# Kernel optimization log

Measured on AMD Instinct MI355X. Metric: run time of the kernel, lower is better.

Reference implementation:

```python
import jax, jax.numpy as jnp
import numpy as np

N = 1048576   # total points
C = 64        # in_planes
B = 16        # number of batch segments
EPS = 1e-5    # BatchNorm eps


def setup_inputs() -> dict:
    key = jax.random.key(0)
    ks = jax.random.split(key, 10)
    x = jax.random.normal(ks[0], (N, C), dtype=jnp.float32)
    # cumulative offsets: equal-size segments, o[-1] == N
    o = (jnp.arange(1, B + 1, dtype=jnp.int32) * (N // B))
    # linear2: Linear(C, C) + ReLU
    W2 = jax.random.normal(ks[1], (C, C), dtype=jnp.float32) / np.sqrt(C)
    b2 = jax.random.normal(ks[2], (C,), dtype=jnp.float32) * 0.01
    # linear1: Linear(2C, C) + BatchNorm1d(C) + ReLU (BN in eval mode)
    W1 = jax.random.normal(ks[3], (2 * C, C), dtype=jnp.float32) / np.sqrt(2 * C)
    b1 = jax.random.normal(ks[4], (C,), dtype=jnp.float32) * 0.01
    gamma = jnp.ones((C,), dtype=jnp.float32)
    beta = jnp.zeros((C,), dtype=jnp.float32)
    run_mean = jax.random.normal(ks[5], (C,), dtype=jnp.float32) * 0.1
    run_var = jax.random.uniform(ks[6], (C,), dtype=jnp.float32, minval=0.5, maxval=1.5)
    return {"x": x, "o": o, "W2": W2, "b2": b2, "W1": W1, "b1": b1,
            "gamma": gamma, "beta": beta, "run_mean": run_mean, "run_var": run_var}


def reference(x, o, W2, b2, W1, b1, gamma, beta, run_mean, run_var):
    n = x.shape[0]
    # segment id of each point from cumulative offsets
    seg = jnp.searchsorted(o, jnp.arange(n, dtype=o.dtype), side="right")  # [N]
    counts = jnp.diff(o, prepend=jnp.zeros((1,), dtype=o.dtype))           # [B]
    # per-segment sum-pool -> mean
    sums = jax.ops.segment_sum(x, seg, num_segments=B)                     # [B, C]
    mean = sums / counts[:, None].astype(x.dtype)                          # [B, C]
    # linear2 + ReLU on the tiny [B, C] pooled features
    h = jax.nn.relu(mean @ W2 + b2)                                        # [B, C]
    # broadcast back to points and concat -> [N, 2C]
    cat = jnp.concatenate([x, h[seg]], axis=1)
    # linear1 + BatchNorm1d (eval mode) + ReLU
    z = cat @ W1 + b1                                                      # [N, C]
    z = (z - run_mean) * jax.lax.rsqrt(run_var + EPS) * gamma + beta
    return jax.nn.relu(z)
```

## Files before the change

kernel.cpp:

```cpp
#include <hip/hip_runtime.h>


#define MAXB 16

typedef _Float16 half8 __attribute__((ext_vector_type(8)));
typedef float float4v __attribute__((ext_vector_type(4)));

__global__ __launch_bounds__(256) void pool_kernel(
    const float* __restrict__ x, const int* __restrict__ o,
    float* __restrict__ gsums, int nB, int ptsPerBlock) {
  __shared__ int so_s[MAXB];
  __shared__ float red[16 * 64];
  __shared__ float ssum2[MAXB * 64];
  const int tid = threadIdx.x;
  if (tid < nB) so_s[tid] = o[tid];
  __syncthreads();

  const int c4 = (tid & 15) * 4;
  const int r  = tid >> 4;
  const int p0 = blockIdx.x * ptsPerBlock;
  const int iters = ptsPerBlock >> 4;

  int sFirst = 0;
  while (p0 >= so_s[sFirst]) sFirst++;
  int sLast = sFirst;
  while (p0 + ptsPerBlock - 1 >= so_s[sLast]) sLast++;

  if (sFirst == sLast) {
    float a0 = 0.f, a1 = 0.f, a2 = 0.f, a3 = 0.f;
    const float* xp = x + (size_t)(p0 + r) * 64 + c4;
#pragma unroll 4
    for (int i = 0; i < iters; ++i) {
      float4 v = *(const float4*)(xp + (size_t)i * 1024);
      a0 += v.x; a1 += v.y; a2 += v.z; a3 += v.w;
    }
    float4 t = {a0, a1, a2, a3};
    *(float4*)&red[r * 64 + c4] = t;
    __syncthreads();
    if (tid < 64) {
      float s = 0.f;
#pragma unroll
      for (int rr = 0; rr < 16; ++rr) s += red[rr * 64 + tid];
      atomicAdd(&gsums[sFirst * 64 + tid], s);
    }
  } else {
    for (int i = tid; i < nB * 64; i += 256) ssum2[i] = 0.f;
    __syncthreads();
    for (int i = 0; i < iters; ++i) {
      int p = p0 + i * 16 + r;
      int s = 0;
      while (p >= so_s[s]) s++;
      float4 v = *(const float4*)(x + (size_t)p * 64 + c4);
      atomicAdd(&ssum2[s * 64 + c4 + 0], v.x);
      atomicAdd(&ssum2[s * 64 + c4 + 1], v.y);
      atomicAdd(&ssum2[s * 64 + c4 + 2], v.z);
      atomicAdd(&ssum2[s * 64 + c4 + 3], v.w);
    }
    __syncthreads();
    for (int i = tid; i < nB * 64; i += 256) {
      float v = ssum2[i];
      if (v != 0.f) atomicAdd(&gsums[i], v);
    }
  }
}

__global__ __launch_bounds__(256) void mid_kernel(
    const float* __restrict__ gsums, const int* __restrict__ o,
    const float* __restrict__ W2, const float* __restrict__ b2,
    const float* __restrict__ W1, const float* __restrict__ b1,
    const float* __restrict__ gamma, const float* __restrict__ beta,
    const float* __restrict__ rmean, const float* __restrict__ rvar,
    float* __restrict__ biasp, _Float16* __restrict__ WpT, int nB) {
  __shared__ float smean[MAXB * 64];
  __shared__ float sh[MAXB * 64];
  const int tid = threadIdx.x;
  const int j = tid & 63;
  const int bq = tid >> 6;

  for (int i = tid; i < nB * 64; i += 256) {
    int b = i >> 6;
    int cnt = o[b] - (b ? o[b - 1] : 0);
    smean[i] = gsums[i] / (float)cnt;
  }
  __syncthreads();

  for (int b = bq; b < nB; b += 4) {
    float p0 = 0.f, p1 = 0.f, p2 = 0.f, p3 = 0.f;
#pragma unroll
    for (int c = 0; c < 64; c += 4) {
      p0 = fmaf(smean[b * 64 + c + 0], W2[(c + 0) * 64 + j], p0);
      p1 = fmaf(smean[b * 64 + c + 1], W2[(c + 1) * 64 + j], p1);
      p2 = fmaf(smean[b * 64 + c + 2], W2[(c + 2) * 64 + j], p2);
      p3 = fmaf(smean[b * 64 + c + 3], W2[(c + 3) * 64 + j], p3);
    }
    sh[b * 64 + j] = fmaxf(((p0 + p1) + (p2 + p3)) + b2[j], 0.f);
  }
  __syncthreads();

  const float a = gamma[j] * rsqrtf(rvar[j] + 1e-5f);
  const float d = beta[j] - rmean[j] * a;
  for (int b = bq; b < nB; b += 4) {
    float p0 = 0.f, p1 = 0.f, p2 = 0.f, p3 = 0.f;
#pragma unroll
    for (int c = 0; c < 64; c += 4) {
      p0 = fmaf(sh[b * 64 + c + 0], W1[(64 + c + 0) * 64 + j], p0);
      p1 = fmaf(sh[b * 64 + c + 1], W1[(64 + c + 1) * 64 + j], p1);
      p2 = fmaf(sh[b * 64 + c + 2], W1[(64 + c + 2) * 64 + j], p2);
      p3 = fmaf(sh[b * 64 + c + 3], W1[(64 + c + 3) * 64 + j], p3);
    }
    biasp[b * 64 + j] = (((p0 + p1) + (p2 + p3)) + b1[j]) * a + d;
  }
  for (int k = bq * 16; k < bq * 16 + 16; ++k)
    WpT[j * 64 + k] = (_Float16)(W1[k * 64 + j] * a);
}

__global__ __launch_bounds__(256) void main_kernel(
    const float* __restrict__ x, const int* __restrict__ o,
    const _Float16* __restrict__ WpT, const float* __restrict__ biasp,
    float* __restrict__ out, int nB) {
  const int lane = threadIdx.x & 63;
  const int m = lane & 15;
  const int quad = lane >> 4;
  const int rows0 = (blockIdx.x * 4 + (threadIdx.x >> 6)) * 128;

  half8 bfrag[4][2];
#pragma unroll
  for (int t = 0; t < 4; ++t)
#pragma unroll
    for (int h = 0; h < 2; ++h)
      bfrag[t][h] = *(const half8*)(WpT + (t * 16 + m) * 64 + h * 32 + quad * 8);

  const int ov = (m < nB) ? o[m] : 0x7fffffff;

  float4 f0, f1, f2, f3;
  {
    const float* p = x + (size_t)(rows0 + m) * 64 + quad * 8;
    f0 = *(const float4*)(p + 0);
    f1 = *(const float4*)(p + 4);
    f2 = *(const float4*)(p + 32);
    f3 = *(const float4*)(p + 36);
  }

  for (int i = 0; i < 8; ++i) {
    const int row0 = rows0 + i * 16;
    half8 a0, a1;
    a0[0] = (_Float16)f0.x; a0[1] = (_Float16)f0.y;
    a0[2] = (_Float16)f0.z; a0[3] = (_Float16)f0.w;
    a0[4] = (_Float16)f1.x; a0[5] = (_Float16)f1.y;
    a0[6] = (_Float16)f1.z; a0[7] = (_Float16)f1.w;
    a1[0] = (_Float16)f2.x; a1[1] = (_Float16)f2.y;
    a1[2] = (_Float16)f2.z; a1[3] = (_Float16)f2.w;
    a1[4] = (_Float16)f3.x; a1[5] = (_Float16)f3.y;
    a1[6] = (_Float16)f3.z; a1[7] = (_Float16)f3.w;

    if (i < 7) {
      const float* p = x + (size_t)(row0 + 16 + m) * 64 + quad * 8;
      f0 = *(const float4*)(p + 0);
      f1 = *(const float4*)(p + 4);
      f2 = *(const float4*)(p + 32);
      f3 = *(const float4*)(p + 36);
    }

    const int s0 = (int)__popcll(__ballot(row0 >= ov) & 0xFFFFull);
    const int s1 = (int)__popcll(__ballot(row0 + 15 >= ov) & 0xFFFFull);

    if (s0 == s1) {
      const float* bp = biasp + s0 * 64 + m;
#pragma unroll
      for (int t = 0; t < 4; ++t) {
        float4v c = {0.f, 0.f, 0.f, 0.f};
        c = __builtin_amdgcn_mfma_f32_16x16x32_f16(a0, bfrag[t][0], c, 0, 0, 0);
        c = __builtin_amdgcn_mfma_f32_16x16x32_f16(a1, bfrag[t][1], c, 0, 0, 0);
        const float bv = bp[t * 16];
        float* op = out + (size_t)(row0 + quad * 4) * 64 + t * 16 + m;
#pragma unroll
        for (int rg = 0; rg < 4; ++rg)
          op[(size_t)rg * 64] = fmaxf(c[rg] + bv, 0.f);
      }
    } else {
#pragma unroll
      for (int t = 0; t < 4; ++t) {
        float4v c = {0.f, 0.f, 0.f, 0.f};
        c = __builtin_amdgcn_mfma_f32_16x16x32_f16(a0, bfrag[t][0], c, 0, 0, 0);
        c = __builtin_amdgcn_mfma_f32_16x16x32_f16(a1, bfrag[t][1], c, 0, 0, 0);
#pragma unroll
        for (int rg = 0; rg < 4; ++rg) {
          const int row = row0 + quad * 4 + rg;
          int s = 0;
          for (int q2 = 0; q2 < nB; ++q2) s += (row >= o[q2]) ? 1 : 0;
          const float bv = biasp[s * 64 + t * 16 + m];
          out[(size_t)row * 64 + t * 16 + m] = fmaxf(c[rg] + bv, 0.f);
        }
      }
    }
  }
}

extern "C" void kernel_launch(void* const* d_in, const int* in_sizes, int n_in,
                              void* d_out, int out_size, void* d_ws, size_t ws_size,
                              hipStream_t stream) {
  const float* x     = (const float*)d_in[0];
  const int*   o     = (const int*)d_in[1];
  const float* W2    = (const float*)d_in[2];
  const float* b2    = (const float*)d_in[3];
  const float* W1    = (const float*)d_in[4];
  const float* b1    = (const float*)d_in[5];
  const float* gamma = (const float*)d_in[6];
  const float* beta  = (const float*)d_in[7];
  const float* rmean = (const float*)d_in[8];
  const float* rvar  = (const float*)d_in[9];
  float* out = (float*)d_out;

  const int npts = in_sizes[0] / 64;
  const int nB   = in_sizes[1];

  float*    gsums = (float*)d_ws;
  float*    biasp = gsums + MAXB * 64;
  _Float16* WpT   = (_Float16*)(biasp + MAXB * 64);

  hipMemsetAsync(gsums, 0, MAXB * 64 * sizeof(float), stream);

  const int blocks1 = 2048;
  pool_kernel<<<blocks1, 256, 0, stream>>>(x, o, gsums, nB, npts / blocks1);
  mid_kernel<<<1, 256, 0, stream>>>(gsums, o, W2, b2, W1, b1, gamma, beta,
                                    rmean, rvar, biasp, WpT, nB);
  main_kernel<<<npts / 512, 256, 0, stream>>>(x, o, WpT, biasp, out, nB);
}
```

Before: 524.7 us.

## Fuse pool, mid and main kernels into one persistent kernel with grid barrier

Merges the three launches into a single 512-block kernel. Each block pools its own chunk of points, then all blocks meet at a global atomic barrier. After the barrier every block redundantly computes the pooled MLP bias into shared memory, builds its own fp16 weight fragments, and then computes its rows. Because each block processes the same points it pooled, the x re-read may hit in L2/MALL, and launch gaps disappear. Output stores become nontemporal. The risks are that the barrier deadlocks if all 512 blocks cannot be co-resident, that parallelism is lower than the earlier 2048-block grid, and that the tiny MLP is repeated in every block.

```diff
diff --git a/kernel.cpp b/kernel.cpp
--- a/kernel.cpp
+++ b/kernel.cpp
@@ -2,23 +2,33 @@
 
 
 #define MAXB 16
+#define NBLK 512
 
 typedef _Float16 half8 __attribute__((ext_vector_type(8)));
 typedef float float4v __attribute__((ext_vector_type(4)));
 
-__global__ __launch_bounds__(256) void pool_kernel(
+__global__ __launch_bounds__(256, 2) void fused_kernel(
     const float* __restrict__ x, const int* __restrict__ o,
-    float* __restrict__ gsums, int nB, int ptsPerBlock) {
+    const float* __restrict__ W2, const float* __restrict__ b2,
+    const float* __restrict__ W1, const float* __restrict__ b1,
+    const float* __restrict__ gamma, const float* __restrict__ beta,
+    const float* __restrict__ rmean, const float* __restrict__ rvar,
+    float* __restrict__ gsums, unsigned* __restrict__ bar,
+    float* __restrict__ out, int nB, int npts) {
   __shared__ int so_s[MAXB];
   __shared__ float red[16 * 64];
-  __shared__ float ssum2[MAXB * 64];
+  __shared__ float sh[MAXB * 64];
+  __shared__ float sbias[MAXB * 64];
+
   const int tid = threadIdx.x;
+  const int ptsPerBlock = npts / NBLK;
+  const int p0 = blockIdx.x * ptsPerBlock;
+
   if (tid < nB) so_s[tid] = o[tid];
   __syncthreads();
 
   const int c4 = (tid & 15) * 4;
   const int r  = tid >> 4;
-  const int p0 = blockIdx.x * ptsPerBlock;
   const int iters = ptsPerBlock >> 4;
 
   int sFirst = 0;
@@ -44,93 +54,97 @@
       atomicAdd(&gsums[sFirst * 64 + tid], s);
     }
   } else {
-    for (int i = tid; i < nB * 64; i += 256) ssum2[i] = 0.f;
+    for (int i = tid; i < nB * 64; i += 256) sh[i] = 0.f;
     __syncthreads();
     for (int i = 0; i < iters; ++i) {
       int p = p0 + i * 16 + r;
       int s = 0;
       while (p >= so_s[s]) s++;
       float4 v = *(const float4*)(x + (size_t)p * 64 + c4);
-      atomicAdd(&ssum2[s * 64 + c4 + 0], v.x);
-      atomicAdd(&ssum2[s * 64 + c4 + 1], v.y);
-      atomicAdd(&ssum2[s * 64 + c4 + 2], v.z);
-      atomicAdd(&ssum2[s * 64 + c4 + 3], v.w);
+      atomicAdd(&sh[s * 64 + c4 + 0], v.x);
+      atomicAdd(&sh[s * 64 + c4 + 1], v.y);
+      atomicAdd(&sh[s * 64 + c4 + 2], v.z);
+      atomicAdd(&sh[s * 64 + c4 + 3], v.w);
     }
     __syncthreads();
     for (int i = tid; i < nB * 64; i += 256) {
-      float v = ssum2[i];
+      float v = sh[i];
       if (v != 0.f) atomicAdd(&gsums[i], v);
     }
-  }
-}
-
-__global__ __launch_bounds__(256) void mid_kernel(
-    const float* __restrict__ gsums, const int* __restrict__ o,
-    const float* __restrict__ W2, const float* __restrict__ b2,
-    const float* __restrict__ W1, const float* __restrict__ b1,
-    const float* __restrict__ gamma, const float* __restrict__ beta,
-    const float* __restrict__ rmean, const float* __restrict__ rvar,
-    float* __restrict__ biasp, _Float16* __restrict__ WpT, int nB) {
-  __shared__ float smean[MAXB * 64];
-  __shared__ float sh[MAXB * 64];
-  const int tid = threadIdx.x;
-  const int j = tid & 63;
+    __syncthreads();
+  }
+
+  const int lane = tid & 63;
+  const int m    = lane & 15;
+  const int quad = lane >> 4;
+  half8 bfrag[4][2];
+#pragma unroll
+  for (int t = 0; t < 4; ++t) {
+    const int jj = t * 16 + m;
+    const float at = gamma[jj] * rsqrtf(rvar[jj] + 1e-5f);
+#pragma unroll
+    for (int h = 0; h < 2; ++h)
+#pragma unroll
+      for (int i2 = 0; i2 < 8; ++i2)
+        bfrag[t][h][i2] = (_Float16)(W1[(h * 32 + quad * 8 + i2) * 64 + jj] * at);
+  }
+
+  __threadfence();
+  __syncthreads();
+  if (tid == 0) {
+    __hip_atomic_fetch_add(bar, 1u, __ATOMIC_ACQ_REL, __HIP_MEMORY_SCOPE_AGENT);
+    while (__hip_atomic_load(bar, __ATOMIC_ACQUIRE, __HIP_MEMORY_SCOPE_AGENT) <
+           (unsigned)NBLK)
+      __builtin_amdgcn_s_sleep(1);
+  }
+  __syncthreads();
+
+  const int j  = tid & 63;
   const int bq = tid >> 6;
-
   for (int i = tid; i < nB * 64; i += 256) {
     int b = i >> 6;
-    int cnt = o[b] - (b ? o[b - 1] : 0);
-    smean[i] = gsums[i] / (float)cnt;
+    int cnt = so_s[b] - (b ? so_s[b - 1] : 0);
+    float g = __hip_atomic_load(&gsums[i], __ATOMIC_RELAXED,
+                                __HIP_MEMORY_SCOPE_AGENT);
+    red[i] = g / (float)cnt;
   }
   __syncthreads();
 
   for (int b = bq; b < nB; b += 4) {
-    float p0 = 0.f, p1 = 0.f, p2 = 0.f, p3 = 0.f;
+    float q0 = 0.f, q1 = 0.f, q2 = 0.f, q3 = 0.f;
 #pragma unroll
     for (int c = 0; c < 64; c += 4) {
-      p0 = fmaf(smean[b * 64 + c + 0], W2[(c + 0) * 64 + j], p0);
-      p1 = fmaf(smean[b * 64 + c + 1], W2[(c + 1) * 64 + j], p1);
-      p2 = fmaf(smean[b * 64 + c + 2], W2[(c + 2) * 64 + j], p2);
-      p3 = fmaf(smean[b * 64 + c + 3], W2[(c + 3) * 64 + j], p3);
-    }
-    sh[b * 64 + j] = fmaxf(((p0 + p1) + (p2 + p3)) + b2[j], 0.f);
-  }
-  __syncthreads();
-
-  const float a = gamma[j] * rsqrtf(rvar[j] + 1e-5f);
-  const float d = beta[j] - rmean[j] * a;
-  for (int b = bq; b < nB; b += 4) {
-    float p0 = 0.f, p1 = 0.f, p2 = 0.f, p3 = 0.f;
-#pragma unroll
-    for (int c = 0; c < 64; c += 4) {
-      p0 = fmaf(sh[b * 64 + c + 0], W1[(64 + c + 0) * 64 + j], p0);
-      p1 = fmaf(sh[b * 64 + c + 1], W1[(64 + c + 1) * 64 + j], p1);
-      p2 = fmaf(sh[b * 64 + c + 2], W1[(64 + c + 2) * 64 + j], p2);
-      p3 = fmaf(sh[b * 64 + c + 3], W1[(64 + c + 3) * 64 + j], p3);
-    }
-    biasp[b * 64 + j] = (((p0 + p1) + (p2 + p3)) + b1[j]) * a + d;
-  }
-  for (int k = bq * 16; k < bq * 16 + 16; ++k)
-    WpT[j * 64 + k] = (_Float16)(W1[k * 64 + j] * a);
-}
-
-__global__ __launch_bounds__(256) void main_kernel(
-    const float* __restrict__ x, const int* __restrict__ o,
-    const _Float16* __restrict__ WpT, const float* __restrict__ biasp,
-    float* __restrict__ out, int nB) {
-  const int lane = threadIdx.x & 63;
-  const int m = lane & 15;
-  const int quad = lane >> 4;
-  const int rows0 = (blockIdx.x * 4 + (threadIdx.x >> 6)) * 128;
-
-  half8 bfrag[4][2];
-#pragma unroll
-  for (int t = 0; t < 4; ++t)
-#pragma unroll
-    for (int h = 0; h < 2; ++h)
-      bfrag[t][h] = *(const half8*)(WpT + (t * 16 + m) * 64 + h * 32 + quad * 8);
-
-  const int ov = (m < nB) ? o[m] : 0x7fffffff;
+      q0 = fmaf(red[b * 64 + c + 0], W2[(c + 0) * 64 + j], q0);
+      q1 = fmaf(red[b * 64 + c + 1], W2[(c + 1) * 64 + j], q1);
+      q2 = fmaf(red[b * 64 + c + 2], W2[(c + 2) * 64 + j], q2);
+      q3 = fmaf(red[b * 64 + c + 3], W2[(c + 3) * 64 + j], q3);
+    }
+    sh[b * 64 + j] = fmaxf(((q0 + q1) + (q2 + q3)) + b2[j], 0.f);
+  }
+  __syncthreads();
+
+  {
+    const float aj = gamma[j] * rsqrtf(rvar[j] + 1e-5f);
+    const float dj = beta[j] - rmean[j] * aj;
+    for (int b = bq; b < nB; b += 4) {
+      float q0 = 0.f, q1 = 0.f, q2 = 0.f, q3 = 0.f;
+#pragma unroll
+      for (int c = 0; c < 64; c += 4) {
+        q0 = fmaf(sh[b * 64 + c + 0], W1[(64 + c + 0) * 64 + j], q0);
+        q1 = fmaf(sh[b * 64 + c + 1], W1[(64 + c + 1) * 64 + j], q1);
+        q2 = fmaf(sh[b * 64 + c + 2], W1[(64 + c + 2) * 64 + j], q2);
+        q3 = fmaf(sh[b * 64 + c + 3], W1[(64 + c + 3) * 64 + j], q3);
+      }
+      sbias[b * 64 + j] = (((q0 + q1) + (q2 + q3)) + b1[j]) * aj + dj;
+    }
+  }
+  __syncthreads();
+
+  const int ov = (m < nB) ? so_s[m] : 0x7fffffff;
+  const int w = tid >> 6;
+  const int wrows = ptsPerBlock >> 2;
+  const int rows0 = p0 + w * wrows;
+  const int ntiles = wrows >> 4;
 
   float4 f0, f1, f2, f3;
   {
@@ -141,7 +155,7 @@
     f3 = *(const float4*)(p + 36);
   }
 
-  for (int i = 0; i < 8; ++i) {
+  for (int i = 0; i < ntiles; ++i) {
     const int row0 = rows0 + i * 16;
     half8 a0, a1;
     a0[0] = (_Float16)f0.x; a0[1] = (_Float16)f0.y;
@@ -153,7 +167,7 @@
     a1[4] = (_Float16)f3.x; a1[5] = (_Float16)f3.y;
     a1[6] = (_Float16)f3.z; a1[7] = (_Float16)f3.w;
 
-    if (i < 7) {
+    if (i < ntiles - 1) {
       const float* p = x + (size_t)(row0 + 16 + m) * 64 + quad * 8;
       f0 = *(const float4*)(p + 0);
       f1 = *(const float4*)(p + 4);
@@ -165,17 +179,17 @@
     const int s1 = (int)__popcll(__ballot(row0 + 15 >= ov) & 0xFFFFull);
 
     if (s0 == s1) {
-      const float* bp = biasp + s0 * 64 + m;
 #pragma unroll
       for (int t = 0; t < 4; ++t) {
         float4v c = {0.f, 0.f, 0.f, 0.f};
         c = __builtin_amdgcn_mfma_f32_16x16x32_f16(a0, bfrag[t][0], c, 0, 0, 0);
         c = __builtin_amdgcn_mfma_f32_16x16x32_f16(a1, bfrag[t][1], c, 0, 0, 0);
-        const float bv = bp[t * 16];
+        const float bv = sbias[s0 * 64 + t * 16 + m];
         float* op = out + (size_t)(row0 + quad * 4) * 64 + t * 16 + m;
 #pragma unroll
         for (int rg = 0; rg < 4; ++rg)
-          op[(size_t)rg * 64] = fmaxf(c[rg] + bv, 0.f);
+          __builtin_nontemporal_store(fmaxf(c[rg] + bv, 0.f),
+                                      op + (size_t)rg * 64);
       }
     } else {
 #pragma unroll
@@ -187,9 +201,10 @@
         for (int rg = 0; rg < 4; ++rg) {
           const int row = row0 + quad * 4 + rg;
           int s = 0;
-          for (int q2 = 0; q2 < nB; ++q2) s += (row >= o[q2]) ? 1 : 0;
-          const float bv = biasp[s * 64 + t * 16 + m];
-          out[(size_t)row * 64 + t * 16 + m] = fmaxf(c[rg] + bv, 0.f);
+          for (int q2 = 0; q2 < nB; ++q2) s += (row >= so_s[q2]) ? 1 : 0;
+          const float bv = sbias[s * 64 + t * 16 + m];
+          __builtin_nontemporal_store(fmaxf(c[rg] + bv, 0.f),
+                                      out + (size_t)row * 64 + t * 16 + m);
         }
       }
     }
@@ -215,14 +230,10 @@
   const int nB   = in_sizes[1];
 
   float*    gsums = (float*)d_ws;
-  float*    biasp = gsums + MAXB * 64;
-  _Float16* WpT   = (_Float16*)(biasp + MAXB * 64);
-
-  hipMemsetAsync(gsums, 0, MAXB * 64 * sizeof(float), stream);
-
-  const int blocks1 = 2048;
-  pool_kernel<<<blocks1, 256, 0, stream>>>(x, o, gsums, nB, npts / blocks1);
-  mid_kernel<<<1, 256, 0, stream>>>(gsums, o, W2, b2, W1, b1, gamma, beta,
-                                    rmean, rvar, biasp, WpT, nB);
-  main_kernel<<<npts / 512, 256, 0, stream>>>(x, o, WpT, biasp, out, nB);
+  unsigned* bar   = (unsigned*)(gsums + MAXB * 64);
+
+  hipMemsetAsync(d_ws, 0, MAXB * 64 * sizeof(float) + 64, stream);
+
+  fused_kernel<<<NBLK, 256, 0, stream>>>(x, o, W2, b2, W1, b1, gamma, beta,
+                                         rmean, rvar, gsums, bar, out, nB, npts);
 }
```

Result: slower. 592.1 us (+12.8%).
